# Performance work log

Measured on AMD Instinct MI355X. Metric: run time of the kernel, lower is better.

The kernel has to match this reference:

```python
import jax, jax.numpy as jnp
import numpy as np

B, N, M, D = 8, 4096, 4096, 3

def setup_inputs() -> dict:
    key = jax.random.key(0)
    ks = jax.random.split(key, 6)
    return {
        "X_pred": jax.random.normal(ks[0], (B, N, D), dtype=jnp.float32),
        "X_true": jax.random.normal(ks[1], (B, M, D), dtype=jnp.float32),
        "R_pred": jax.random.normal(ks[2], (B, D, D), dtype=jnp.float32),
        "t_pred": jax.random.normal(ks[3], (B, D), dtype=jnp.float32),
        "R_true": jax.random.normal(ks[4], (B, D, D), dtype=jnp.float32),
        "t_true": jax.random.normal(ks[5], (B, D), dtype=jnp.float32),
        "temperature": jnp.asarray(0.1, dtype=jnp.float32),
    }

def reference(X_pred, X_true, R_pred, t_pred, R_true, t_true, temperature):
    # Rigid transforms: x' = R x + t
    Xp = jnp.einsum('bij,bnj->bni', R_pred, X_pred) + t_pred[:, None, :]  # (B,N,D)
    Xt = jnp.einsum('bij,bmj->bmi', R_true, X_true) + t_true[:, None, :]  # (B,M,D)
    # Squared pairwise distances: |a|^2 + |b|^2 - 2 a.b  (== cdist(p=2)**2)
    sq_p = jnp.sum(Xp * Xp, axis=-1)  # (B,N)
    sq_t = jnp.sum(Xt * Xt, axis=-1)  # (B,M)
    dist_sq = sq_p[:, :, None] + sq_t[:, None, :] - 2.0 * jnp.einsum('bnd,bmd->bnm', Xp, Xt)
    dist_sq = jnp.maximum(dist_sq, 0.0)  # (B,N,M)
    soft_alignment = jax.nn.softmax(-dist_sq / temperature, axis=-1)
    weighted_distances = jnp.sum(soft_alignment * dist_sq, axis=-1)  # (B,N)
    return jnp.mean(weighted_distances)
```

## Files before the change

kernel.cpp:

```cpp
#include <hip/hip_runtime.h>


#define B_    8
#define N_    4096
#define M_    4096
#define NWAVE 8
#define BLOCK (NWAVE * 64)
#define ROWS  512
#define MSPL  8
#define QCH   (M_ / MSPL)
#define WQ    (QCH / NWAVE)
#define LOG2E 1.4426950408889634f
#define LN2   0.6931471805599453f
#define BIGF  3.0e38f

typedef float v2f __attribute__((ext_vector_type(2)));

__global__ __launch_bounds__(BLOCK, 6) void softfape_main(
    const float* __restrict__ X_pred, const float* __restrict__ X_true,
    const float* __restrict__ R_pred, const float* __restrict__ t_pred,
    const float* __restrict__ R_true, const float* __restrict__ t_true,
    const float* __restrict__ temp,
    float4* __restrict__ Pg)
{
    __shared__ float4 Q[QCH];
    __shared__ float  MLp[NWAVE][ROWS];
    __shared__ float  Sp[NWAVE][ROWS];
    __shared__ float  shl[ROWS];
    __shared__ float  pwl[ROWS];

    const int tid  = threadIdx.x;
    const int wave = tid >> 6;
    const int lane = tid & 63;
    const int x    = blockIdx.x;
    const int ms   = x & 7;
    const int rg   = (x >> 3) & 7;
    const int b    = x >> 6;

    const float T   = temp[0];
    const float c   = LOG2E / T;
    const float m2c = -2.0f * c;

    if (tid < QCH / 2) {
        const float g00 = R_true[b*9+0], g01 = R_true[b*9+1], g02 = R_true[b*9+2];
        const float g10 = R_true[b*9+3], g11 = R_true[b*9+4], g12 = R_true[b*9+5];
        const float g20 = R_true[b*9+6], g21 = R_true[b*9+7], g22 = R_true[b*9+8];
        const float u0  = t_true[b*3+0], u1 = t_true[b*3+1], u2 = t_true[b*3+2];
        const float2* xt = (const float2*)(X_true + ((size_t)b * M_ + ms * QCH) * 3);
        const float2 f0 = xt[3*tid+0], f1 = xt[3*tid+1], f2 = xt[3*tid+2];
        {
            const float y0 = fmaf(g00, f0.x, fmaf(g01, f0.y, fmaf(g02, f1.x, u0)));
            const float y1 = fmaf(g10, f0.x, fmaf(g11, f0.y, fmaf(g12, f1.x, u1)));
            const float y2 = fmaf(g20, f0.x, fmaf(g21, f0.y, fmaf(g22, f1.x, u2)));
            const float nn = fmaf(y0, y0, fmaf(y1, y1, y2 * y2));
            Q[2*tid]   = make_float4(m2c*y0, m2c*y1, m2c*y2, c*nn);
        }
        {
            const float y0 = fmaf(g00, f1.y, fmaf(g01, f2.x, fmaf(g02, f2.y, u0)));
            const float y1 = fmaf(g10, f1.y, fmaf(g11, f2.x, fmaf(g12, f2.y, u1)));
            const float y2 = fmaf(g20, f1.y, fmaf(g21, f2.x, fmaf(g22, f2.y, u2)));
            const float nn = fmaf(y0, y0, fmaf(y1, y1, y2 * y2));
            Q[2*tid+1] = make_float4(m2c*y0, m2c*y1, m2c*y2, c*nn);
        }
    }

    v2f px2[4], py2[4], pz2[4];
    {
        const float h00 = R_pred[b*9+0], h01 = R_pred[b*9+1], h02 = R_pred[b*9+2];
        const float h10 = R_pred[b*9+3], h11 = R_pred[b*9+4], h12 = R_pred[b*9+5];
        const float h20 = R_pred[b*9+6], h21 = R_pred[b*9+7], h22 = R_pred[b*9+8];
        const float v0 = t_pred[b*3+0], v1 = t_pred[b*3+1], v2 = t_pred[b*3+2];
        const float4* xp = (const float4*)(X_pred + ((size_t)b * N_ + rg * ROWS + lane * 8) * 3);
        const float4 a0 = xp[0], a1 = xp[1], a2 = xp[2];
        const float4 a3 = xp[3], a4 = xp[4], a5 = xp[5];
        const float rx[8] = {a0.x, a0.w, a1.z, a2.y, a3.x, a3.w, a4.z, a5.y};
        const float ry[8] = {a0.y, a1.x, a1.w, a2.z, a3.y, a4.x, a4.w, a5.z};
        const float rz[8] = {a0.z, a1.y, a2.x, a2.w, a3.z, a4.y, a5.x, a5.w};
        #pragma unroll
        for (int j = 0; j < 8; ++j) {
            const float ppx = fmaf(h00, rx[j], fmaf(h01, ry[j], fmaf(h02, rz[j], v0)));
            const float ppy = fmaf(h10, rx[j], fmaf(h11, ry[j], fmaf(h12, rz[j], v1)));
            const float ppz = fmaf(h20, rx[j], fmaf(h21, ry[j], fmaf(h22, rz[j], v2)));
            px2[j >> 1][j & 1] = ppx;
            py2[j >> 1][j & 1] = ppy;
            pz2[j >> 1][j & 1] = ppz;
            pwl[8*lane + j] = c * fmaf(ppx, ppx, fmaf(ppy, ppy, ppz * ppz));
        }
    }

    __syncthreads();

    const float4* __restrict__ Qw = Q + wave * WQ;

    v2f mA2[4] = {{BIGF, BIGF}, {BIGF, BIGF}, {BIGF, BIGF}, {BIGF, BIGF}};
    #pragma unroll 4
    for (int k = 0; k < WQ; ++k) {
        const float4 q = Qw[k];
        const v2f qx = {q.x, q.x}, qy = {q.y, q.y}, qz = {q.z, q.z}, qw = {q.w, q.w};
        #pragma unroll
        for (int j = 0; j < 4; ++j) {
            const v2f A = qx * px2[j] + (qy * py2[j] + (qz * pz2[j] + qw));
            mA2[j] = __builtin_elementwise_min(mA2[j], A);
        }
    }
    #pragma unroll
    for (int j = 0; j < 4; ++j) {
        MLp[wave][8*lane + 2*j]     = mA2[j].x;
        MLp[wave][8*lane + 2*j + 1] = mA2[j].y;
    }
    __syncthreads();

    {
        float m = MLp[0][tid];
        #pragma unroll
        for (int w2 = 1; w2 < NWAVE; ++w2) m = fminf(m, MLp[w2][tid]);
        shl[tid] = m;
    }
    __syncthreads();

    v2f sh2[4];
    {
        const float4 s0 = *(const float4*)&shl[8*lane];
        const float4 s1 = *(const float4*)&shl[8*lane + 4];
        sh2[0] = (v2f){s0.x, s0.y};  sh2[1] = (v2f){s0.z, s0.w};
        sh2[2] = (v2f){s1.x, s1.y};  sh2[3] = (v2f){s1.z, s1.w};
    }

    v2f L2[4]  = {{0.f,0.f},{0.f,0.f},{0.f,0.f},{0.f,0.f}};
    v2f SA2[4] = {{0.f,0.f},{0.f,0.f},{0.f,0.f},{0.f,0.f}};
    #pragma unroll 4
    for (int k = 0; k < WQ; ++k) {
        const float4 q = Qw[k];
        const v2f qx = {q.x, q.x}, qy = {q.y, q.y}, qz = {q.z, q.z}, qw = {q.w, q.w};
        #pragma unroll
        for (int j = 0; j < 4; ++j) {
            const v2f A   = qx * px2[j] + (qy * py2[j] + (qz * pz2[j] + qw));
            const v2f arg = sh2[j] - A;
            const v2f w   = {__builtin_amdgcn_exp2f(arg.x),
                             __builtin_amdgcn_exp2f(arg.y)};
            L2[j]  += w;
            SA2[j]  = w * arg + SA2[j];
        }
    }
    #pragma unroll
    for (int j = 0; j < 4; ++j) {
        MLp[wave][8*lane + 2*j]     = L2[j].x;
        MLp[wave][8*lane + 2*j + 1] = L2[j].y;
        Sp[wave][8*lane + 2*j]      = SA2[j].x;
        Sp[wave][8*lane + 2*j + 1]  = SA2[j].y;
    }
    __syncthreads();

    {
        float Lr = 0.0f, Sr = 0.0f;
        #pragma unroll
        for (int w2 = 0; w2 < NWAVE; ++w2) { Lr += MLp[w2][tid]; Sr += Sp[w2][tid]; }
        const size_t row = (size_t)b * N_ + rg * ROWS + tid;
        Pg[row * MSPL + ms] = make_float4(shl[tid] + pwl[tid], Lr, Sr, 0.0f);
    }
}

__global__ __launch_bounds__(256) void softfape_finalize(
    const float4* __restrict__ Pg, const float* __restrict__ temp,
    float* __restrict__ out)
{
    __shared__ float ws4[4];
    const int tid = threadIdx.x;
    const size_t row = (size_t)blockIdx.x * 256 + tid;

    float4 P[MSPL];
    #pragma unroll
    for (int i = 0; i < MSPL; ++i) P[i] = Pg[row * MSPL + i];

    float m = P[0].x;
    #pragma unroll
    for (int i = 1; i < MSPL; ++i) m = fminf(m, P[i].x);

    float L = 0.0f, SA = 0.0f;
    #pragma unroll
    for (int i = 0; i < MSPL; ++i) {
        const float dm = m - P[i].x;
        const float f  = __builtin_amdgcn_exp2f(dm);
        L  = fmaf(P[i].y, f, L);
        SA = fmaf(f, fmaf(dm, P[i].y, P[i].z), SA);
    }
    float wd = m - SA / L;

    wd += __shfl_xor(wd, 1);  wd += __shfl_xor(wd, 2);  wd += __shfl_xor(wd, 4);
    wd += __shfl_xor(wd, 8);  wd += __shfl_xor(wd, 16); wd += __shfl_xor(wd, 32);
    if ((tid & 63) == 0) ws4[tid >> 6] = wd;
    __syncthreads();
    if (tid == 0) {
        const float s = ws4[0] + ws4[1] + ws4[2] + ws4[3];
        const float scale = temp[0] * LN2 / ((float)B_ * (float)N_);
        atomicAdd(out, s * scale);
    }
}

extern "C" void kernel_launch(void* const* d_in, const int* in_sizes, int n_in,
                              void* d_out, int out_size, void* d_ws, size_t ws_size,
                              hipStream_t stream) {
    const float* X_pred = (const float*)d_in[0];
    const float* X_true = (const float*)d_in[1];
    const float* R_pred = (const float*)d_in[2];
    const float* t_pred = (const float*)d_in[3];
    const float* R_true = (const float*)d_in[4];
    const float* t_true = (const float*)d_in[5];
    const float* temp   = (const float*)d_in[6];
    float* out = (float*)d_out;

    float4* Pg = (float4*)d_ws;

    hipMemsetAsync(out, 0, sizeof(float), stream);

    softfape_main<<<dim3(B_ * 8 * MSPL), BLOCK, 0, stream>>>(
        X_pred, X_true, R_pred, t_pred, R_true, t_true, temp, Pg);

    softfape_finalize<<<dim3((B_ * N_) / 256), 256, 0, stream>>>(Pg, temp, out);
}
```

Measured before the change: 105.3 us.

## Split M across 16 chunks, shrink LDS scratch, transpose partial layout

Doubles the M-split so the grid has twice as many blocks, each with a smaller Q chunk. One shared scratch array is now reused for the L and S reductions so more blocks fit per CU, and launch bounds are raised to 8. The partial results are stored chunk-major so finalize reads them coalesced. In exchange there are more partials to merge, extra barriers, and the Q staging and min pass are repeated per block.

```diff
diff --git a/kernel.cpp b/kernel.cpp
--- a/kernel.cpp
+++ b/kernel.cpp
@@ -7,7 +7,7 @@
 #define NWAVE 8
 #define BLOCK (NWAVE * 64)
 #define ROWS  512
-#define MSPL  8
+#define MSPL  16
 #define QCH   (M_ / MSPL)
 #define WQ    (QCH / NWAVE)
 #define LOG2E 1.4426950408889634f
@@ -16,7 +16,7 @@
 
 typedef float v2f __attribute__((ext_vector_type(2)));
 
-__global__ __launch_bounds__(BLOCK, 6) void softfape_main(
+__global__ __launch_bounds__(BLOCK, 8) void softfape_main(
     const float* __restrict__ X_pred, const float* __restrict__ X_true,
     const float* __restrict__ R_pred, const float* __restrict__ t_pred,
     const float* __restrict__ R_true, const float* __restrict__ t_true,
@@ -24,8 +24,7 @@
     float4* __restrict__ Pg)
 {
     __shared__ float4 Q[QCH];
-    __shared__ float  MLp[NWAVE][ROWS];
-    __shared__ float  Sp[NWAVE][ROWS];
+    __shared__ float  Wp[NWAVE][ROWS];
     __shared__ float  shl[ROWS];
     __shared__ float  pwl[ROWS];
 
@@ -33,9 +32,9 @@
     const int wave = tid >> 6;
     const int lane = tid & 63;
     const int x    = blockIdx.x;
-    const int ms   = x & 7;
-    const int rg   = (x >> 3) & 7;
-    const int b    = x >> 6;
+    const int ms   = x & 15;
+    const int rg   = (x >> 4) & 7;
+    const int b    = x >> 7;
 
     const float T   = temp[0];
     const float c   = LOG2E / T;
@@ -84,7 +83,7 @@
             px2[j >> 1][j & 1] = ppx;
             py2[j >> 1][j & 1] = ppy;
             pz2[j >> 1][j & 1] = ppz;
-            pwl[8*lane + j] = c * fmaf(ppx, ppx, fmaf(ppy, ppy, ppz * ppz));
+            if (wave == 0) pwl[8*lane + j] = c * fmaf(ppx, ppx, fmaf(ppy, ppy, ppz * ppz));
         }
     }
 
@@ -105,15 +104,15 @@
     }
     #pragma unroll
     for (int j = 0; j < 4; ++j) {
-        MLp[wave][8*lane + 2*j]     = mA2[j].x;
-        MLp[wave][8*lane + 2*j + 1] = mA2[j].y;
-    }
-    __syncthreads();
-
-    {
-        float m = MLp[0][tid];
-        #pragma unroll
-        for (int w2 = 1; w2 < NWAVE; ++w2) m = fminf(m, MLp[w2][tid]);
+        Wp[wave][8*lane + 2*j]     = mA2[j].x;
+        Wp[wave][8*lane + 2*j + 1] = mA2[j].y;
+    }
+    __syncthreads();
+
+    {
+        float m = Wp[0][tid];
+        #pragma unroll
+        for (int w2 = 1; w2 < NWAVE; ++w2) m = fminf(m, Wp[w2][tid]);
         shl[tid] = m;
     }
     __syncthreads();
@@ -142,21 +141,30 @@
             SA2[j]  = w * arg + SA2[j];
         }
     }
+
     #pragma unroll
     for (int j = 0; j < 4; ++j) {
-        MLp[wave][8*lane + 2*j]     = L2[j].x;
-        MLp[wave][8*lane + 2*j + 1] = L2[j].y;
-        Sp[wave][8*lane + 2*j]      = SA2[j].x;
-        Sp[wave][8*lane + 2*j + 1]  = SA2[j].y;
-    }
-    __syncthreads();
-
-    {
-        float Lr = 0.0f, Sr = 0.0f;
-        #pragma unroll
-        for (int w2 = 0; w2 < NWAVE; ++w2) { Lr += MLp[w2][tid]; Sr += Sp[w2][tid]; }
+        Wp[wave][8*lane + 2*j]     = L2[j].x;
+        Wp[wave][8*lane + 2*j + 1] = L2[j].y;
+    }
+    __syncthreads();
+    float Lr = 0.0f;
+    #pragma unroll
+    for (int w2 = 0; w2 < NWAVE; ++w2) Lr += Wp[w2][tid];
+    __syncthreads();
+    #pragma unroll
+    for (int j = 0; j < 4; ++j) {
+        Wp[wave][8*lane + 2*j]     = SA2[j].x;
+        Wp[wave][8*lane + 2*j + 1] = SA2[j].y;
+    }
+    __syncthreads();
+    float Sr = 0.0f;
+    #pragma unroll
+    for (int w2 = 0; w2 < NWAVE; ++w2) Sr += Wp[w2][tid];
+
+    {
         const size_t row = (size_t)b * N_ + rg * ROWS + tid;
-        Pg[row * MSPL + ms] = make_float4(shl[tid] + pwl[tid], Lr, Sr, 0.0f);
+        Pg[(size_t)ms * (B_ * N_) + row] = make_float4(shl[tid] + pwl[tid], Lr, Sr, 0.0f);
     }
 }
 
@@ -170,7 +178,7 @@
 
     float4 P[MSPL];
     #pragma unroll
-    for (int i = 0; i < MSPL; ++i) P[i] = Pg[row * MSPL + i];
+    for (int i = 0; i < MSPL; ++i) P[i] = Pg[(size_t)i * (B_ * N_) + row];
 
     float m = P[0].x;
     #pragma unroll
```

Result: slower. 211.2 us (+100.5%).
